# Performance work log

Hardware: AMD Instinct MI355X
Metric: run time of the kernel (lower is better)

Reference implementation:

```python
import jax, jax.numpy as jnp
import numpy as np

N = 40962  # icosphere level-6 vertex count
EPS = 1e-5

def setup_inputs() -> dict:
    key = jax.random.key(0)
    ks = jax.random.split(key, 8)
    x = jax.random.normal(ks[0], (N, 3), dtype=jnp.float32)
    neigh_orders = jax.random.randint(ks[1], (N * 7,), 0, N, dtype=jnp.int32)
    s0 = 1.0 / np.sqrt(21.0)
    sm = 1.0 / np.sqrt(896.0)
    return {
        "x": x,
        "neigh_orders": neigh_orders,
        "W0": jax.random.uniform(ks[2], (21, 128), jnp.float32, -s0, s0),
        "b0": jax.random.uniform(ks[3], (128,), jnp.float32, -s0, s0),
        "g0": jnp.ones((128,), jnp.float32),
        "be0": jnp.zeros((128,), jnp.float32),
        "Wm": jax.random.uniform(ks[4], (14, 896, 128), jnp.float32, -sm, sm),
        "bm": jax.random.uniform(ks[5], (14, 128), jnp.float32, -sm, sm),
        "gm": jnp.ones((14, 128), jnp.float32),
        "bem": jnp.zeros((14, 128), jnp.float32),
        "Wl": jax.random.uniform(ks[6], (896, 36), jnp.float32, -sm, sm),
        "bl": jax.random.uniform(ks[7], (36,), jnp.float32, -sm, sm),
    }

def _bs(x, idx, W, b):
    # gather 7 fixed ring neighbors per node, flatten, dense linear
    mat = x[idx].reshape(x.shape[0], -1)  # [N, 7*in_feats]
    return mat @ W + b

def _bn_train(h, g, be):
    # BatchNorm1d in training mode: biased variance over the node/batch dim
    mu = jnp.mean(h, axis=0)
    var = jnp.var(h, axis=0)
    return g * (h - mu) * jax.lax.rsqrt(var + EPS) + be

def reference(x, neigh_orders, W0, b0, g0, be0, Wm, bm, gm, bem, Wl, bl):
    idx = neigh_orders
    h = jax.nn.relu(_bn_train(_bs(x, idx, W0, b0), g0, be0))  # [N, 128]

    def step(h, params):
        W, b, g, be = params
        h = jax.nn.relu(_bn_train(_bs(h, idx, W, b), g, be))
        return h, None

    h, _ = jax.lax.scan(step, h, (Wm, bm, gm, bem))  # 14 identical 128->128 blocks
    out = _bs(h, idx, Wl, bl)  # [N, num_classes]
    return out
```

## Files before the change

kernel.cpp:

```cpp
#include <hip/hip_runtime.h>

typedef _Float16 f16x8 __attribute__((ext_vector_type(8)));
typedef float f32x4 __attribute__((ext_vector_type(4)));

#define EPS 1e-5f

__device__ __forceinline__ short f2h(float x) {
    _Float16 h = (_Float16)x;
    union { _Float16 h; short s; } u;
    u.h = h;
    return u.s;
}

__global__ void prep_kernel(const float* __restrict__ Wm, const float* __restrict__ Wl,
                            short* __restrict__ WtM, short* __restrict__ WtF,
                            float* __restrict__ stats) {
    const long T1 = 14L * 896 * 128;
    const long T2 = 48L * 896;
    const long T3 = 15L * 256;
    long i = (long)blockIdx.x * blockDim.x + threadIdx.x;
    if (i < T1) {
        long l = i / (896 * 128);
        long r = i % (896 * 128);
        long k = r >> 7;
        long f = r & 127;
        WtM[l * 114688 + f * 896 + k] = f2h(Wm[i]);
    } else if (i < T1 + T2) {
        long j = i - T1;
        long f = j / 896;
        long k = j % 896;
        WtF[j] = (f < 36) ? f2h(Wl[k * 36 + f]) : (short)0;
    } else if (i < T1 + T2 + T3) {
        stats[i - T1 - T2] = 0.0f;
    }
}

#define L0_NB 16
__global__ __launch_bounds__(256) void layer0_kernel(
        const float* __restrict__ x, const int* __restrict__ idx,
        const float* __restrict__ W0, const float* __restrict__ b0,
        short* __restrict__ hlin, float* __restrict__ stats, int N) {
    __shared__ float sX[L0_NB * 21];
    __shared__ float sStat[256];
    const int tid = threadIdx.x;
    const int f = tid & 127;
    const int half = tid >> 7;
    float wreg[21];
#pragma unroll
    for (int k = 0; k < 21; ++k) wreg[k] = W0[k * 128 + f];
    const float bf = b0[f];
    float s = 0.f, ss = 0.f;
    const int ntiles = (N + L0_NB - 1) / L0_NB;
    const int gs = gridDim.x;

    const int e0 = tid;
    const int ni0 = e0 / 21, k0e = e0 - ni0 * 21;
    const int j0 = k0e / 3, c0 = k0e - j0 * 3;
    const int e1 = tid + 256;
    const int ni1 = e1 / 21, k1e = e1 - ni1 * 21;
    const int j1 = k1e / 3, c1 = k1e - j1 * 3;

    auto issueX = [&](int t, float& a0, float& a1) {
        if (t >= ntiles) return;
        const int base = t * L0_NB;
        int n = base + ni0; if (n >= N) n = N - 1;
        a0 = x[(long)idx[n * 7 + j0] * 3 + c0];
        if (tid < 80) {
            int n2 = base + ni1; if (n2 >= N) n2 = N - 1;
            a1 = x[(long)idx[n2 * 7 + j1] * 3 + c1];
        }
    };

    float cx0 = 0.f, cx1 = 0.f, nx0 = 0.f, nx1 = 0.f;
    issueX(blockIdx.x, cx0, cx1);

    for (int t = blockIdx.x; t < ntiles; t += gs) {
        const int n0 = t * L0_NB;
        __syncthreads();
        sX[e0] = cx0;
        if (tid < 80) sX[e1] = cx1;
        issueX(t + gs, nx0, nx1);
        __syncthreads();
#pragma unroll
        for (int ni = 0; ni < 8; ++ni) {
            int node = n0 + half * 8 + ni;
            if (node >= N) break;
            float acc = bf;
#pragma unroll
            for (int k = 0; k < 21; ++k)
                acc = fmaf(sX[(half * 8 + ni) * 21 + k], wreg[k], acc);
            hlin[(long)node * 128 + f] = f2h(acc);
            s += acc;
            ss += acc * acc;
        }
        cx0 = nx0; cx1 = nx1;
    }
    __syncthreads();
    if (half == 1) { sStat[f] = s; sStat[128 + f] = ss; }
    __syncthreads();
    if (half == 0) {
        atomicAdd(&stats[f], s + sStat[f]);
        atomicAdd(&stats[128 + f], ss + sStat[128 + f]);
    }
}

__global__ __launch_bounds__(256, 4) void gemm_mid_kernel(
        const short* __restrict__ hprev, const int* __restrict__ idx,
        const short* __restrict__ Wt, const float* __restrict__ bvec,
        const float* __restrict__ g, const float* __restrict__ be,
        const float* __restrict__ statsIn,
        short* __restrict__ hlin, float* __restrict__ statsOut,
        int N, float invN) {
    __shared__ short sA[64 * 136];
    __shared__ short sB[64 * 136];
    __shared__ float sAux[256];

    const int tid = threadIdx.x;
    const int wave = tid >> 6;
    const int lane = tid & 63;
    const int quad = lane >> 4;
    const int l16 = lane & 15;
    const int wm = wave & 1;
    const int wf = wave >> 1;
    const int tile = blockIdx.x >> 1;
    const int fg = blockIdx.x & 1;
    const int m0 = tile * 64;
    const int f0 = fg * 64;
    const int t16 = tid >> 4;
    const int fb = (tid & 15) * 8;

    if (tid < 128) {
        float mu = statsIn[tid] * invN;
        float var = statsIn[128 + tid] * invN - mu * mu;
        float rs = rsqrtf(var + EPS);
        float sc = g[tid] * rs;
        sAux[tid] = sc;
        sAux[128 + tid] = be[tid] - mu * sc;
    }
    __syncthreads();
    float scR[8], shR[8];
#pragma unroll
    for (int e = 0; e < 8; ++e) {
        scR[e] = sAux[fb + e];
        shR[e] = sAux[128 + fb + e];
    }

    f32x4 acc[2][2];
#pragma unroll
    for (int ni = 0; ni < 2; ++ni) {
        float bv0 = bvec[f0 + wf * 32 + ni * 16 + l16];
#pragma unroll
        for (int mi = 0; mi < 2; ++mi) {
            acc[mi][ni][0] = bv0; acc[mi][ni][1] = bv0; acc[mi][ni][2] = bv0; acc[mi][ni][3] = bv0;
        }
    }

    f16x8 av[4];
    f16x8 bv[4];

    auto issueA = [&](int j) {
#pragma unroll
        for (int it = 0; it < 4; ++it) {
            int nl = t16 + it * 16;
            int n = m0 + nl;
            n = (n < N) ? n : (N - 1);
            long row = idx[n * 7 + j];
            av[it] = *(const f16x8*)&hprev[row * 128 + fb];
        }
    };
    auto issueB = [&](int j) {
#pragma unroll
        for (int it = 0; it < 4; ++it) {
            int ff = f0 + t16 + it * 16;
            bv[it] = *(const f16x8*)&Wt[(long)ff * 896 + j * 128 + fb];
        }
    };
    auto writeA = [&]() {
#pragma unroll
        for (int it = 0; it < 4; ++it) {
            int nl = t16 + it * 16;
            f16x8 hv = av[it];
            union { short sh8[8]; f16x8 v; } u;
#pragma unroll
            for (int e = 0; e < 8; ++e) {
                float v = (float)hv[e];
                u.sh8[e] = f2h(fmaxf(fmaf(v, scR[e], shR[e]), 0.f));
            }
            *(f16x8*)&sA[nl * 136 + fb] = u.v;
        }
    };
    auto writeB = [&]() {
#pragma unroll
        for (int it = 0; it < 4; ++it) {
            int ffl = t16 + it * 16;
            *(f16x8*)&sB[ffl * 136 + fb] = bv[it];
        }
    };

    issueB(0);
    issueA(0);

    for (int j = 0; j < 7; ++j) {
        __syncthreads();
        writeB();
        writeA();
        if (j < 6) {
            issueB(j + 1);
            issueA(j + 1);
        }
        __syncthreads();
#pragma unroll
        for (int k0 = 0; k0 < 128; k0 += 32) {
            f16x8 a[2], b[2];
#pragma unroll
            for (int mi = 0; mi < 2; ++mi)
                a[mi] = *(const f16x8*)&sA[(wm * 32 + mi * 16 + l16) * 136 + k0 + quad * 8];
#pragma unroll
            for (int ni = 0; ni < 2; ++ni)
                b[ni] = *(const f16x8*)&sB[(wf * 32 + ni * 16 + l16) * 136 + k0 + quad * 8];
#pragma unroll
            for (int mi = 0; mi < 2; ++mi)
#pragma unroll
                for (int ni = 0; ni < 2; ++ni)
                    acc[mi][ni] = __builtin_amdgcn_mfma_f32_16x16x32_f16(a[mi], b[ni], acc[mi][ni], 0, 0, 0);
        }
    }

    __syncthreads();
    if (tid < 128) sAux[tid] = 0.f;
    __syncthreads();
#pragma unroll
    for (int ni = 0; ni < 2; ++ni) {
        int lf = wf * 32 + ni * 16 + l16;
        float s = 0.f, ss = 0.f;
#pragma unroll
        for (int mi = 0; mi < 2; ++mi) {
#pragma unroll
            for (int r = 0; r < 4; ++r) {
                int node = m0 + wm * 32 + mi * 16 + quad * 4 + r;
                float v = acc[mi][ni][r];
                if (node < N) {
                    hlin[(long)node * 128 + f0 + lf] = f2h(v);
                    s += v;
                    ss += v * v;
                }
            }
        }
        atomicAdd(&sAux[lf], s);
        atomicAdd(&sAux[64 + lf], ss);
    }
    __syncthreads();
    if (tid < 64) {
        atomicAdd(&statsOut[f0 + tid], sAux[tid]);
        atomicAdd(&statsOut[128 + f0 + tid], sAux[64 + tid]);
    }
}

__global__ __launch_bounds__(256) void gemm_final_kernel(
        const short* __restrict__ hprev, const int* __restrict__ idx,
        const short* __restrict__ WtF, const float* __restrict__ bl,
        const float* __restrict__ g, const float* __restrict__ be,
        const float* __restrict__ statsIn,
        float* __restrict__ out, int N, float invN) {
    __shared__ short sA[64 * 136];
    __shared__ short sB[48 * 136];
    __shared__ float sAux[256];

    const int tid = threadIdx.x;
    const int wave = tid >> 6;
    const int lane = tid & 63;
    const int quad = lane >> 4;
    const int l16 = lane & 15;
    const int m0 = blockIdx.x * 64;
    const int t16 = tid >> 4;
    const int fb = (tid & 15) * 8;

    if (tid < 128) {
        float mu = statsIn[tid] * invN;
        float var = statsIn[128 + tid] * invN - mu * mu;
        float rs = rsqrtf(var + EPS);
        float sc = g[tid] * rs;
        sAux[tid] = sc;
        sAux[128 + tid] = be[tid] - mu * sc;
    }
    __syncthreads();
    float scR[8], shR[8];
#pragma unroll
    for (int e = 0; e < 8; ++e) {
        scR[e] = sAux[fb + e];
        shR[e] = sAux[128 + fb + e];
    }

    f32x4 acc[3];
#pragma unroll
    for (int ni = 0; ni < 3; ++ni) {
        int feat = ni * 16 + l16;
        float bv0 = (feat < 36) ? bl[feat] : 0.f;
        acc[ni][0] = bv0; acc[ni][1] = bv0; acc[ni][2] = bv0; acc[ni][3] = bv0;
    }

    f16x8 av[4];
    f16x8 bv[3];

    auto issueA = [&](int j) {
#pragma unroll
        for (int it = 0; it < 4; ++it) {
            int nl = t16 + it * 16;
            int n = m0 + nl;
            n = (n < N) ? n : (N - 1);
            long row = idx[n * 7 + j];
            av[it] = *(const f16x8*)&hprev[row * 128 + fb];
        }
    };
    auto issueB = [&](int j) {
#pragma unroll
        for (int it = 0; it < 3; ++it) {
            int ff = t16 + it * 16;
            bv[it] = *(const f16x8*)&WtF[(long)ff * 896 + j * 128 + fb];
        }
    };
    auto writeA = [&]() {
#pragma unroll
        for (int it = 0; it < 4; ++it) {
            int nl = t16 + it * 16;
            f16x8 hv = av[it];
            union { short sh8[8]; f16x8 v; } u;
#pragma unroll
            for (int e = 0; e < 8; ++e) {
                float v = (float)hv[e];
                u.sh8[e] = f2h(fmaxf(fmaf(v, scR[e], shR[e]), 0.f));
            }
            *(f16x8*)&sA[nl * 136 + fb] = u.v;
        }
    };
    auto writeB = [&]() {
#pragma unroll
        for (int it = 0; it < 3; ++it) {
            int ff = t16 + it * 16;
            *(f16x8*)&sB[ff * 136 + fb] = bv[it];
        }
    };

    issueB(0);
    issueA(0);

    for (int j = 0; j < 7; ++j) {
        __syncthreads();
        writeB();
        writeA();
        if (j < 6) {
            issueB(j + 1);
            issueA(j + 1);
        }
        __syncthreads();
#pragma unroll
        for (int k0 = 0; k0 < 128; k0 += 32) {
            f16x8 a = *(const f16x8*)&sA[(wave * 16 + l16) * 136 + k0 + quad * 8];
            f16x8 b[3];
#pragma unroll
            for (int ni = 0; ni < 3; ++ni)
                b[ni] = *(const f16x8*)&sB[(ni * 16 + l16) * 136 + k0 + quad * 8];
#pragma unroll
            for (int ni = 0; ni < 3; ++ni)
                acc[ni] = __builtin_amdgcn_mfma_f32_16x16x32_f16(a, b[ni], acc[ni], 0, 0, 0);
        }
    }

#pragma unroll
    for (int ni = 0; ni < 3; ++ni) {
        int feat = ni * 16 + l16;
        if (feat < 36) {
#pragma unroll
            for (int r = 0; r < 4; ++r) {
                int node = m0 + wave * 16 + quad * 4 + r;
                if (node < N) out[(long)node * 36 + feat] = acc[ni][r];
            }
        }
    }
}

extern "C" void kernel_launch(void* const* d_in, const int* in_sizes, int n_in,
                              void* d_out, int out_size, void* d_ws, size_t ws_size,
                              hipStream_t stream) {
    const float* x   = (const float*)d_in[0];
    const int*   idx = (const int*)d_in[1];
    const float* W0  = (const float*)d_in[2];
    const float* b0  = (const float*)d_in[3];
    const float* g0  = (const float*)d_in[4];
    const float* be0 = (const float*)d_in[5];
    const float* Wm  = (const float*)d_in[6];
    const float* bm  = (const float*)d_in[7];
    const float* gm  = (const float*)d_in[8];
    const float* bem = (const float*)d_in[9];
    const float* Wl  = (const float*)d_in[10];
    const float* bl  = (const float*)d_in[11];
    float* out = (float*)d_out;

    const int N = in_sizes[0] / 3;
    const float invN = 1.0f / (float)N;

    char* ws = (char*)d_ws;
    size_t off = 0;
    auto alloc = [&](size_t bytes) -> void* {
        void* p = ws + off;
        off = (off + bytes + 255) & ~(size_t)255;
        return p;
    };
    short* WtM   = (short*)alloc(14UL * 128 * 896 * 2);
    short* WtF   = (short*)alloc(48UL * 896 * 2);
    float* stats = (float*)alloc(15UL * 256 * 4);
    short* hlinA = (short*)alloc((size_t)N * 128 * 2);
    short* hlinB = (short*)alloc((size_t)N * 128 * 2);

    {
        long total = 14L * 896 * 128 + 48L * 896 + 15L * 256;
        int blocks = (int)((total + 255) / 256);
        prep_kernel<<<blocks, 256, 0, stream>>>(Wm, Wl, WtM, WtF, stats);
    }

    layer0_kernel<<<1280, 256, 0, stream>>>(x, idx, W0, b0, hlinA, stats, N);

    const int gblocks_mid = ((N + 63) / 64) * 2;
    short* hin = hlinA;
    short* hout = hlinB;
    const float* gPrev = g0;
    const float* bePrev = be0;
    for (int L = 0; L < 14; ++L) {
        gemm_mid_kernel<<<gblocks_mid, 256, 0, stream>>>(
            hin, idx, WtM + (size_t)L * 128 * 896, bm + L * 128,
            gPrev, bePrev, stats + L * 256,
            hout, stats + (L + 1) * 256, N, invN);
        gPrev = gm + L * 128;
        bePrev = bem + L * 128;
        short* t = hin; hin = hout; hout = t;
    }

    const int gblocks_fin = (N + 63) / 64;
    gemm_final_kernel<<<gblocks_fin, 256, 0, stream>>>(
        hin, idx, WtF, bl, gm + 13 * 128, bem + 13 * 128, stats + 14 * 256,
        out, N, invN);
}
```

Baseline: 607.2 us.

## Prefetch gathered neighbor rows two stages ahead with sched barriers

The gather GEMM kernels now keep two register buffers of gathered activation rows, so loads for neighbor j+2 are issued while j is being written to LDS and j+1 waits in registers. The 7-step loop is fully unrolled, with sched_barrier calls that stop the compiler from sinking the global loads past the barriers. The aim is to hide gather latency behind MFMA work. It costs more VGPRs, and the final kernel gets a launch_bounds occupancy hint of 4 that could force spills.

```diff
diff --git a/kernel.cpp b/kernel.cpp
--- a/kernel.cpp
+++ b/kernel.cpp
@@ -80,6 +80,7 @@
         sX[e0] = cx0;
         if (tid < 80) sX[e1] = cx1;
         issueX(t + gs, nx0, nx1);
+        __builtin_amdgcn_sched_barrier(0);
         __syncthreads();
 #pragma unroll
         for (int ni = 0; ni < 8; ++ni) {
@@ -155,10 +156,10 @@
         }
     }
 
-    f16x8 av[4];
+    f16x8 av0[4], av1[4];
     f16x8 bv[4];
 
-    auto issueA = [&](int j) {
+    auto issueA = [&](int j, f16x8 (&av)[4]) {
 #pragma unroll
         for (int it = 0; it < 4; ++it) {
             int nl = t16 + it * 16;
@@ -175,7 +176,7 @@
             bv[it] = *(const f16x8*)&Wt[(long)ff * 896 + j * 128 + fb];
         }
     };
-    auto writeA = [&]() {
+    auto writeA = [&](const f16x8 (&av)[4]) {
 #pragma unroll
         for (int it = 0; it < 4; ++it) {
             int nl = t16 + it * 16;
@@ -196,19 +197,7 @@
             *(f16x8*)&sB[ffl * 136 + fb] = bv[it];
         }
     };
-
-    issueB(0);
-    issueA(0);
-
-    for (int j = 0; j < 7; ++j) {
-        __syncthreads();
-        writeB();
-        writeA();
-        if (j < 6) {
-            issueB(j + 1);
-            issueA(j + 1);
-        }
-        __syncthreads();
+    auto mfma = [&]() {
 #pragma unroll
         for (int k0 = 0; k0 < 128; k0 += 32) {
             f16x8 a[2], b[2];
@@ -224,7 +213,33 @@
                 for (int ni = 0; ni < 2; ++ni)
                     acc[mi][ni] = __builtin_amdgcn_mfma_f32_16x16x32_f16(a[mi], b[ni], acc[mi][ni], 0, 0, 0);
         }
-    }
+    };
+
+    issueB(0);
+    issueA(0, av0);
+    issueA(1, av1);
+    __builtin_amdgcn_sched_barrier(0);
+
+    __syncthreads(); writeB(); writeA(av0);
+    issueB(1); issueA(2, av0); __builtin_amdgcn_sched_barrier(0);
+    __syncthreads(); mfma();
+    __syncthreads(); writeB(); writeA(av1);
+    issueB(2); issueA(3, av1); __builtin_amdgcn_sched_barrier(0);
+    __syncthreads(); mfma();
+    __syncthreads(); writeB(); writeA(av0);
+    issueB(3); issueA(4, av0); __builtin_amdgcn_sched_barrier(0);
+    __syncthreads(); mfma();
+    __syncthreads(); writeB(); writeA(av1);
+    issueB(4); issueA(5, av1); __builtin_amdgcn_sched_barrier(0);
+    __syncthreads(); mfma();
+    __syncthreads(); writeB(); writeA(av0);
+    issueB(5); issueA(6, av0); __builtin_amdgcn_sched_barrier(0);
+    __syncthreads(); mfma();
+    __syncthreads(); writeB(); writeA(av1);
+    issueB(6); __builtin_amdgcn_sched_barrier(0);
+    __syncthreads(); mfma();
+    __syncthreads(); writeB(); writeA(av0);
+    __syncthreads(); mfma();
 
     __syncthreads();
     if (tid < 128) sAux[tid] = 0.f;
@@ -256,7 +271,7 @@
     }
 }
 
-__global__ __launch_bounds__(256) void gemm_final_kernel(
+__global__ __launch_bounds__(256, 4) void gemm_final_kernel(
         const short* __restrict__ hprev, const int* __restrict__ idx,
         const short* __restrict__ WtF, const float* __restrict__ bl,
         const float* __restrict__ g, const float* __restrict__ be,
@@ -299,10 +314,10 @@
         acc[ni][0] = bv0; acc[ni][1] = bv0; acc[ni][2] = bv0; acc[ni][3] = bv0;
     }
 
-    f16x8 av[4];
+    f16x8 av0[4], av1[4];
     f16x8 bv[3];
 
-    auto issueA = [&](int j) {
+    auto issueA = [&](int j, f16x8 (&av)[4]) {
 #pragma unroll
         for (int it = 0; it < 4; ++it) {
             int nl = t16 + it * 16;
@@ -319,7 +334,7 @@
             bv[it] = *(const f16x8*)&WtF[(long)ff * 896 + j * 128 + fb];
         }
     };
-    auto writeA = [&]() {
+    auto writeA = [&](const f16x8 (&av)[4]) {
 #pragma unroll
         for (int it = 0; it < 4; ++it) {
             int nl = t16 + it * 16;
@@ -340,19 +355,7 @@
             *(f16x8*)&sB[ff * 136 + fb] = bv[it];
         }
     };
-
-    issueB(0);
-    issueA(0);
-
-    for (int j = 0; j < 7; ++j) {
-        __syncthreads();
-        writeB();
-        writeA();
-        if (j < 6) {
-            issueB(j + 1);
-            issueA(j + 1);
-        }
-        __syncthreads();
+    auto mfma = [&]() {
 #pragma unroll
         for (int k0 = 0; k0 < 128; k0 += 32) {
             f16x8 a = *(const f16x8*)&sA[(wave * 16 + l16) * 136 + k0 + quad * 8];
@@ -364,7 +367,33 @@
             for (int ni = 0; ni < 3; ++ni)
                 acc[ni] = __builtin_amdgcn_mfma_f32_16x16x32_f16(a, b[ni], acc[ni], 0, 0, 0);
         }
-    }
+    };
+
+    issueB(0);
+    issueA(0, av0);
+    issueA(1, av1);
+    __builtin_amdgcn_sched_barrier(0);
+
+    __syncthreads(); writeB(); writeA(av0);
+    issueB(1); issueA(2, av0); __builtin_amdgcn_sched_barrier(0);
+    __syncthreads(); mfma();
+    __syncthreads(); writeB(); writeA(av1);
+    issueB(2); issueA(3, av1); __builtin_amdgcn_sched_barrier(0);
+    __syncthreads(); mfma();
+    __syncthreads(); writeB(); writeA(av0);
+    issueB(3); issueA(4, av0); __builtin_amdgcn_sched_barrier(0);
+    __syncthreads(); mfma();
+    __syncthreads(); writeB(); writeA(av1);
+    issueB(4); issueA(5, av1); __builtin_amdgcn_sched_barrier(0);
+    __syncthreads(); mfma();
+    __syncthreads(); writeB(); writeA(av0);
+    issueB(5); issueA(6, av0); __builtin_amdgcn_sched_barrier(0);
+    __syncthreads(); mfma();
+    __syncthreads(); writeB(); writeA(av1);
+    issueB(6); __builtin_amdgcn_sched_barrier(0);
+    __syncthreads(); mfma();
+    __syncthreads(); writeB(); writeA(av0);
+    __syncthreads(); mfma();
 
 #pragma unroll
     for (int ni = 0; ni < 3; ++ni) {
```

New measurement: 670.5 us. 1.1x slower.
